# Kernel tuning notes

Measured on AMD Instinct MI355X. Metric: run time of the kernel, lower is better.

The kernel has to match this reference:

```python
import jax, jax.numpy as jnp
import numpy as np

B, N, C = 2, 2048, 1024
H = 16
D = C // H  # head_dim = 64
SCALE = D ** -0.5


def setup_inputs() -> dict:
    key = jax.random.key(0)
    k1, k2, k3, k4 = jax.random.split(key, 4)
    x = jax.random.normal(k1, (B, N, C), dtype=jnp.float32)
    # nn.Linear(in_dim, 3*out_dim, bias=False): store as [in, 3*out] for x @ W
    w_qkv = jax.random.normal(k2, (C, 3 * C), dtype=jnp.float32) * (C ** -0.5)
    w_proj = jax.random.normal(k3, (C, C), dtype=jnp.float32) * (C ** -0.5)
    b_proj = jax.random.normal(k4, (C,), dtype=jnp.float32) * 0.01
    return {"x": x, "w_qkv": w_qkv, "w_proj": w_proj, "b_proj": b_proj}


def reference(x, w_qkv, w_proj, b_proj):
    b, n, c = x.shape
    # QKV projection -> [3, B, H, N, D]
    qkv = (x @ w_qkv).reshape(b, n, 3, H, D).transpose(2, 0, 3, 1, 4)
    q, k, v = qkv[0], qkv[1], qkv[2]
    # scaled dot-product attention, full [B, H, N, N] scores as in original
    attn = jax.nn.softmax(jnp.einsum('bhqd,bhkd->bhqk', q * SCALE, k), axis=-1)
    out = jnp.einsum('bhqk,bhkd->bhqd', attn, v)  # [B, H, N, D]
    out = out.transpose(0, 2, 1, 3).reshape(b, n, c)
    return out @ w_proj + b_proj
```

## Files before the change

kernel.cpp:

```cpp
#include <hip/hip_runtime.h>

typedef unsigned short u16;
typedef float f32x4 __attribute__((ext_vector_type(4)));
typedef short bf16x8 __attribute__((ext_vector_type(8)));
typedef u16 u16x4 __attribute__((ext_vector_type(4)));
typedef u16 u16x8 __attribute__((ext_vector_type(8)));
typedef __bf16 bfr4 __attribute__((ext_vector_type(4)));

#define BB 2
#define NN 2048
#define CC 1024
#define HH 16
#define DD 64
#define MM (BB * NN)
#define NQKV (3 * CC)
#define QSCALE 0.18033688011112042f

#if __has_builtin(__builtin_amdgcn_exp2f)
#define EXP2(x) __builtin_amdgcn_exp2f(x)
#else
#define EXP2(x) exp2f(x)
#endif

__device__ __forceinline__ u16 f2bf(float f) {
    unsigned u = __float_as_uint(f);
    u += 0x7FFFu + ((u >> 16) & 1u);
    return (u16)(u >> 16);
}
__device__ __forceinline__ float bf2f(u16 b) {
    return __uint_as_float(((unsigned)b) << 16);
}

__device__ __forceinline__ void ld_lds16(const u16* g, u16* l) {
    __builtin_amdgcn_global_load_lds(
        (const __attribute__((address_space(1))) unsigned int*)g,
        (__attribute__((address_space(3))) unsigned int*)l, 16, 0, 0);
}

__global__ __launch_bounds__(256) void k_tobf(const float* __restrict__ in,
                                              u16* __restrict__ out, int n) {
    int i = (blockIdx.x * 256 + threadIdx.x) * 8;
    if (i >= n) return;
    float4 a = *(const float4*)(in + i);
    float4 b = *(const float4*)(in + i + 4);
    u16x8 o;
    o[0] = f2bf(a.x); o[1] = f2bf(a.y); o[2] = f2bf(a.z); o[3] = f2bf(a.w);
    o[4] = f2bf(b.x); o[5] = f2bf(b.y); o[6] = f2bf(b.z); o[7] = f2bf(b.w);
    *(u16x8*)(out + i) = o;
}

__global__ __launch_bounds__(256) void k_tcast(const float* __restrict__ in,
                                               u16* __restrict__ out,
                                               int K, int Nn) {
    __shared__ float tile[32][33];
    int t = threadIdx.x, tx = t & 31, ty = t >> 5;
    int n0 = blockIdx.x * 32, k0 = blockIdx.y * 32;
#pragma unroll
    for (int r = 0; r < 32; r += 8)
        tile[ty + r][tx] = in[(size_t)(k0 + ty + r) * Nn + n0 + tx];
    __syncthreads();
#pragma unroll
    for (int r = 0; r < 32; r += 8)
        out[(size_t)(n0 + ty + r) * K + k0 + tx] = f2bf(tile[tx][ty + r]);
}

template <int MODE>
__global__ __launch_bounds__(256) void k_gemm(
    const u16* __restrict__ A, const u16* __restrict__ B,
    u16* __restrict__ Qb, u16* __restrict__ Kb, u16* __restrict__ Vb,
    const float* __restrict__ bias, float* __restrict__ Cout) {
    const int Kd = 1024;
    __shared__ __align__(16) u16 Ah[128][32];
    __shared__ __align__(16) u16 Bh[128][32];

    int t = threadIdx.x;
    int wave = t >> 6, lane = t & 63;
    int quad = lane >> 4, l16 = lane & 15;
    int wm = (wave >> 1) * 64, wn = (wave & 1) * 64;
    int m0 = blockIdx.y * 128, n0 = blockIdx.x * 128;

    int strow0 = wave * 16 + (lane >> 2);
    int stdst  = (lane & 3) * 8;
    int stsrc  = ((lane & 3) ^ ((lane >> 3) & 3)) * 8;
    int cfrag = (quad ^ ((l16 >> 1) & 3)) * 8;

    f32x4 acc[4][4];
#pragma unroll
    for (int i = 0; i < 4; i++)
#pragma unroll
        for (int j = 0; j < 4; j++) acc[i][j] = f32x4{0.f, 0.f, 0.f, 0.f};

    for (int k0 = 0; k0 < Kd; k0 += 32) {
        __syncthreads();
#pragma unroll
        for (int ii = 0; ii < 2; ii++) {
            int row = strow0 + ii * 64;
            ld_lds16(A + (size_t)(m0 + row) * Kd + k0 + stsrc, &Ah[row][stdst]);
            ld_lds16(B + (size_t)(n0 + row) * Kd + k0 + stsrc, &Bh[row][stdst]);
        }
        __syncthreads();

        bf16x8 af[4], bf[4];
#pragma unroll
        for (int i = 0; i < 4; i++) {
            af[i] = *(const bf16x8*)&Ah[wm + i * 16 + l16][cfrag];
            bf[i] = *(const bf16x8*)&Bh[wn + i * 16 + l16][cfrag];
        }
#pragma unroll
        for (int mi = 0; mi < 4; mi++)
#pragma unroll
            for (int ni = 0; ni < 4; ni++)
                acc[mi][ni] = __builtin_amdgcn_mfma_f32_16x16x32_bf16(
                    af[mi], bf[ni], acc[mi][ni], 0, 0, 0);
    }

#pragma unroll
    for (int mi = 0; mi < 4; mi++)
#pragma unroll
        for (int ni = 0; ni < 4; ni++)
#pragma unroll
            for (int r = 0; r < 4; r++) {
                int grow = m0 + wm + mi * 16 + quad * 4 + r;
                int gcol = n0 + wn + ni * 16 + l16;
                float v = acc[mi][ni][r];
                if (MODE == 0) {
                    int three = gcol >> 10, rem = gcol & 1023;
                    int h = rem >> 6, d = rem & 63;
                    int bb = grow >> 11, nn = grow & 2047;
                    if (three == 0) {
                        Qb[((size_t)(bb * HH + h) * NN + nn) * DD + d] = f2bf(v * QSCALE);
                    } else if (three == 1) {
                        Kb[((size_t)(bb * HH + h) * NN + nn) * DD + d] = f2bf(v);
                    } else {
                        Vb[((size_t)(bb * HH + h) * DD + d) * NN + nn] = f2bf(v);
                    }
                } else {
                    Cout[(size_t)grow * CC + gcol] = v + bias[gcol];
                }
            }
}

__global__ __launch_bounds__(256) void k_attn(const u16* __restrict__ Qb,
                                              const u16* __restrict__ Kb,
                                              const u16* __restrict__ VbT,
                                              u16* __restrict__ Opart,
                                              float* __restrict__ Lpart) {
    __shared__ __align__(16) u16 Ks[64][64];
    __shared__ __align__(16) u16 Vs[64][64];
    __shared__ __align__(16) u16 Ps[4][32][64];

    int t = threadIdx.x, wave = t >> 6, lane = t & 63;
    int quad = lane >> 4, l16 = lane & 15;
    int bh = blockIdx.y, sp = blockIdx.z;
    int q0 = blockIdx.x * 128 + wave * 32;
    const size_t kbase = (size_t)bh * NN * DD;
    const size_t vbase = (size_t)bh * DD * NN;

    bf16x8 qf[2][2];
#pragma unroll
    for (int qj = 0; qj < 2; qj++) {
        int qrow = q0 + qj * 16 + l16;
        qf[qj][0] = *(const bf16x8*)&Qb[kbase + (size_t)qrow * DD + quad * 8];
        qf[qj][1] = *(const bf16x8*)&Qb[kbase + (size_t)qrow * DD + 32 + quad * 8];
    }

    bf16x8 ones;
#pragma unroll
    for (int j = 0; j < 8; j++) ones[j] = (short)0x3F80;

    f32x4 o[4][2];
    f32x4 accl[2];
#pragma unroll
    for (int i = 0; i < 4; i++)
#pragma unroll
        for (int j = 0; j < 2; j++) o[i][j] = f32x4{0.f, 0.f, 0.f, 0.f};
    accl[0] = f32x4{0.f, 0.f, 0.f, 0.f};
    accl[1] = f32x4{0.f, 0.f, 0.f, 0.f};

    int stgrp  = lane & 7;
    int stsrc  = (stgrp ^ (lane >> 3)) * 8;
    int strow0 = wave * 16 + (lane >> 3);
    int cf0 = (quad ^ (l16 & 7)) * 8;
    int cf1 = ((4 + quad) ^ (l16 & 7)) * 8;
    int psw = (quad & 1) * 4;

    for (int c = sp * 16; c < sp * 16 + 16; c++) {
        __syncthreads();
#pragma unroll
        for (int ii = 0; ii < 2; ii++) {
            int row = strow0 + ii * 8;
            ld_lds16(&Kb[kbase + (size_t)(c * 64 + row) * DD + stsrc], &Ks[row][stgrp * 8]);
            ld_lds16(&VbT[vbase + (size_t)row * NN + c * 64 + stsrc], &Vs[row][stgrp * 8]);
        }
        __syncthreads();

        bf16x8 kf[4][2];
#pragma unroll
        for (int kt = 0; kt < 4; kt++) {
            kf[kt][0] = *(const bf16x8*)&Ks[kt * 16 + l16][cf0];
            kf[kt][1] = *(const bf16x8*)&Ks[kt * 16 + l16][cf1];
        }

#pragma unroll
        for (int qj = 0; qj < 2; qj++) {
            f32x4 s[4];
#pragma unroll
            for (int kt = 0; kt < 4; kt++) {
                f32x4 z = f32x4{0.f, 0.f, 0.f, 0.f};
                z = __builtin_amdgcn_mfma_f32_16x16x32_bf16(kf[kt][0], qf[qj][0], z, 0, 0, 0);
                z = __builtin_amdgcn_mfma_f32_16x16x32_bf16(kf[kt][1], qf[qj][1], z, 0, 0, 0);
                s[kt] = z;
            }
#pragma unroll
            for (int kt = 0; kt < 4; kt++) {
                bfr4 pk;
#pragma unroll
                for (int r = 0; r < 4; r++) pk[r] = (__bf16)EXP2(s[kt][r]);
                int og = 2 * kt + (quad >> 1);
                *(bfr4*)&Ps[wave][qj * 16 + l16][(og ^ (l16 & 7)) * 8 + psw] = pk;
            }
        }
        __asm__ volatile("s_waitcnt lgkmcnt(0)" ::: "memory");

        bf16x8 pb[2][2];
#pragma unroll
        for (int qj = 0; qj < 2; qj++) {
            pb[qj][0] = *(const bf16x8*)&Ps[wave][qj * 16 + l16][cf0];
            pb[qj][1] = *(const bf16x8*)&Ps[wave][qj * 16 + l16][cf1];
            accl[qj] = __builtin_amdgcn_mfma_f32_16x16x32_bf16(ones, pb[qj][0], accl[qj], 0, 0, 0);
            accl[qj] = __builtin_amdgcn_mfma_f32_16x16x32_bf16(ones, pb[qj][1], accl[qj], 0, 0, 0);
        }
#pragma unroll
        for (int dt = 0; dt < 4; dt++) {
            bf16x8 vf0 = *(const bf16x8*)&Vs[dt * 16 + l16][cf0];
            bf16x8 vf1 = *(const bf16x8*)&Vs[dt * 16 + l16][cf1];
#pragma unroll
            for (int qj = 0; qj < 2; qj++) {
                o[dt][qj] = __builtin_amdgcn_mfma_f32_16x16x32_bf16(vf0, pb[qj][0], o[dt][qj], 0, 0, 0);
                o[dt][qj] = __builtin_amdgcn_mfma_f32_16x16x32_bf16(vf1, pb[qj][1], o[dt][qj], 0, 0, 0);
            }
        }
    }

    int b = bh >> 4, h = bh & 15;
#pragma unroll
    for (int qj = 0; qj < 2; qj++) {
        int grow = b * NN + q0 + qj * 16 + l16;
        size_t orow = ((size_t)sp * MM + grow) * CC;
#pragma unroll
        for (int dt = 0; dt < 4; dt++) {
            u16x4 hv;
#pragma unroll
            for (int r = 0; r < 4; r++) hv[r] = f2bf(o[dt][qj][r]);
            *(u16x4*)&Opart[orow + h * DD + dt * 16 + quad * 4] = hv;
        }
        if (quad == 0)
            Lpart[((size_t)sp * MM + grow) * HH + h] = accl[qj][0];
    }
}

__global__ __launch_bounds__(256) void k_reduce(const u16* __restrict__ Op,
                                                const float* __restrict__ Lp,
                                                u16* __restrict__ Ob) {
    size_t i = ((size_t)blockIdx.x * 256 + threadIdx.x) * 8;
    int m = (int)(i >> 10);
    int c = (int)(i & 1023);
    int h = c >> 6;
    float l = Lp[(size_t)m * HH + h] + Lp[(size_t)(MM + m) * HH + h];
    float inv = 1.f / l;
    u16x8 p0 = *(const u16x8*)&Op[i];
    u16x8 p1 = *(const u16x8*)&Op[(size_t)MM * CC + i];
    u16x8 o;
#pragma unroll
    for (int j = 0; j < 8; j++) o[j] = f2bf((bf2f(p0[j]) + bf2f(p1[j])) * inv);
    *(u16x8*)&Ob[i] = o;
}

extern "C" void kernel_launch(void* const* d_in, const int* in_sizes, int n_in,
                              void* d_out, int out_size, void* d_ws, size_t ws_size,
                              hipStream_t stream) {
    const float* x      = (const float*)d_in[0];
    const float* w_qkv  = (const float*)d_in[1];
    const float* w_proj = (const float*)d_in[2];
    const float* b_proj = (const float*)d_in[3];
    float* out = (float*)d_out;

    u16* p = (u16*)d_ws;
    u16* Xb = p; p += (size_t)MM * CC;
    u16* Wq = p; p += (size_t)NQKV * CC;
    u16* Wp = p; p += (size_t)CC * CC;
    u16* Qb = p; p += (size_t)MM * CC;
    u16* Kb = p; p += (size_t)MM * CC;
    u16* Vb = p; p += (size_t)MM * CC;
    u16* Ob = p; p += (size_t)MM * CC;
    u16* Opart = p; p += (size_t)2 * MM * CC;
    float* Lpart = (float*)p;

    k_tobf<<<(MM * CC) / (256 * 8), 256, 0, stream>>>(x, Xb, MM * CC);
    k_tcast<<<dim3(NQKV / 32, CC / 32), 256, 0, stream>>>(w_qkv, Wq, CC, NQKV);
    k_tcast<<<dim3(CC / 32, CC / 32), 256, 0, stream>>>(w_proj, Wp, CC, CC);
    k_gemm<0><<<dim3(NQKV / 128, MM / 128), 256, 0, stream>>>(
        Xb, Wq, Qb, Kb, Vb, nullptr, nullptr);
    k_attn<<<dim3(NN / 128, BB * HH, 2), 256, 0, stream>>>(Qb, Kb, Vb, Opart, Lpart);
    k_reduce<<<(MM * CC) / (256 * 8), 256, 0, stream>>>(Opart, Lpart, Ob);
    k_gemm<1><<<dim3(CC / 128, MM / 128), 256, 0, stream>>>(
        Ob, Wp, nullptr, nullptr, nullptr, b_proj, out);
}
```

Baseline: 208.9 us.

## Double-buffer K/V tiles in LDS to overlap loads with attention compute

K and V shared-memory tiles become two-stage ping-pong buffers. The first chunk is loaded before the loop. Each iteration then issues the global-to-LDS load for the next chunk right after the barrier and computes on the current buffer, which also drops one of the two barriers per iteration. The goal is to hide global load latency behind the MFMA and exp work. The cost is doubled K/V LDS usage, which may reduce occupancy, and correctness relies on the barrier draining the outstanding async loads.

Measured after the change: 207.4 us. Within noise of the previous version (-0.7%).

```diff
diff --git a/kernel.cpp b/kernel.cpp
--- a/kernel.cpp
+++ b/kernel.cpp
@@ -145,8 +145,8 @@
                                               const u16* __restrict__ VbT,
                                               u16* __restrict__ Opart,
                                               float* __restrict__ Lpart) {
-    __shared__ __align__(16) u16 Ks[64][64];
-    __shared__ __align__(16) u16 Vs[64][64];
+    __shared__ __align__(16) u16 Ks[2][64][64];
+    __shared__ __align__(16) u16 Vs[2][64][64];
     __shared__ __align__(16) u16 Ps[4][32][64];
 
     int t = threadIdx.x, wave = t >> 6, lane = t & 63;
@@ -184,21 +184,33 @@
     int cf1 = ((4 + quad) ^ (l16 & 7)) * 8;
     int psw = (quad & 1) * 4;
 
-    for (int c = sp * 16; c < sp * 16 + 16; c++) {
+    const int c0 = sp * 16;
+
+#pragma unroll
+    for (int ii = 0; ii < 2; ii++) {
+        int row = strow0 + ii * 8;
+        ld_lds16(&Kb[kbase + (size_t)(c0 * 64 + row) * DD + stsrc], &Ks[0][row][stgrp * 8]);
+        ld_lds16(&VbT[vbase + (size_t)row * NN + c0 * 64 + stsrc], &Vs[0][row][stgrp * 8]);
+    }
+
+    for (int i = 0; i < 16; i++) {
         __syncthreads();
-#pragma unroll
-        for (int ii = 0; ii < 2; ii++) {
-            int row = strow0 + ii * 8;
-            ld_lds16(&Kb[kbase + (size_t)(c * 64 + row) * DD + stsrc], &Ks[row][stgrp * 8]);
-            ld_lds16(&VbT[vbase + (size_t)row * NN + c * 64 + stsrc], &Vs[row][stgrp * 8]);
-        }
-        __syncthreads();
+        if (i < 15) {
+            int c = c0 + i + 1, nb = (i + 1) & 1;
+#pragma unroll
+            for (int ii = 0; ii < 2; ii++) {
+                int row = strow0 + ii * 8;
+                ld_lds16(&Kb[kbase + (size_t)(c * 64 + row) * DD + stsrc], &Ks[nb][row][stgrp * 8]);
+                ld_lds16(&VbT[vbase + (size_t)row * NN + c * 64 + stsrc], &Vs[nb][row][stgrp * 8]);
+            }
+        }
+        const int bi = i & 1;
 
         bf16x8 kf[4][2];
 #pragma unroll
         for (int kt = 0; kt < 4; kt++) {
-            kf[kt][0] = *(const bf16x8*)&Ks[kt * 16 + l16][cf0];
-            kf[kt][1] = *(const bf16x8*)&Ks[kt * 16 + l16][cf1];
+            kf[kt][0] = *(const bf16x8*)&Ks[bi][kt * 16 + l16][cf0];
+            kf[kt][1] = *(const bf16x8*)&Ks[bi][kt * 16 + l16][cf1];
         }
 
 #pragma unroll
@@ -232,8 +244,8 @@
         }
 #pragma unroll
         for (int dt = 0; dt < 4; dt++) {
-            bf16x8 vf0 = *(const bf16x8*)&Vs[dt * 16 + l16][cf0];
-            bf16x8 vf1 = *(const bf16x8*)&Vs[dt * 16 + l16][cf1];
+            bf16x8 vf0 = *(const bf16x8*)&Vs[bi][dt * 16 + l16][cf0];
+            bf16x8 vf1 = *(const bf16x8*)&Vs[bi][dt * 16 + l16][cf1];
 #pragma unroll
             for (int qj = 0; qj < 2; qj++) {
                 o[dt][qj] = __builtin_amdgcn_mfma_f32_16x16x32_bf16(vf0, pb[qj][0], o[dt][qj], 0, 0, 0);
```
